# Performance work log

Hardware: AMD Instinct MI355X
Metric: run time of the kernel (lower is better)

## Reference

```python
import jax, jax.numpy as jnp
import numpy as np

VOCAB = 50000
EMBED = 512
COMP = 300
B, L = 2048, 200
CENTER = jnp.array([40.7127, -74.0059], dtype=jnp.float32)


def setup_inputs() -> dict:
    key = jax.random.key(0)
    ks = jax.random.split(key, 8)
    words = jax.random.randint(ks[0], (B, L), 0, VOCAB, dtype=jnp.int64)
    features = jax.random.normal(ks[1], (B, 2), dtype=jnp.float32)
    mask = jnp.ones((B, L), dtype=jnp.float32)
    # nn.Linear(vocab_size, embedding_dim): weight [out, in]
    lim1 = 1.0 / np.sqrt(VOCAB)
    W_hidden = jax.random.uniform(ks[2], (EMBED, VOCAB), jnp.float32, -lim1, lim1)
    b_hidden = jax.random.uniform(ks[3], (EMBED,), jnp.float32, -lim1, lim1)
    lim2 = 1.0 / np.sqrt(EMBED)
    W_pi = jax.random.uniform(ks[4], (COMP, EMBED), jnp.float32, -lim2, lim2)
    b_pi = jax.random.uniform(ks[5], (COMP,), jnp.float32, -lim2, lim2)
    # mu = (rand-0.5)*4 + CENTER ; sigma = rand * log(0.01)
    mu = (jax.random.uniform(ks[6], (COMP, 2), jnp.float32) - 0.5) * 4.0 + CENTER
    sigma = jax.random.uniform(ks[7], (COMP, 2), jnp.float32) * np.log(0.01).astype(np.float32)
    return {"words": words, "features": features, "mask": mask,
            "W_hidden": W_hidden, "b_hidden": b_hidden,
            "W_pi": W_pi, "b_pi": b_pi, "mu": mu, "sigma": sigma}


def reference(words, features, mask, W_hidden, b_hidden, W_pi, b_pi, mu, sigma):
    bsz = words.shape[0]
    # binary bag-of-words one-hot: s[words[i]] = 1 (duplicates collapse to 1)
    q = jnp.zeros((bsz, VOCAB), dtype=W_hidden.dtype)
    q = q.at[jnp.arange(bsz)[:, None], words].set(1.0)
    hidden = jnp.tanh(q @ W_hidden.T + b_hidden)          # [B, E]
    pi = jax.nn.softmax(hidden @ W_pi.T + b_pi, axis=-1).T  # [C, B]
    sigma_out = jnp.exp(sigma)                             # [C, 2]
    return pi, sigma_out, mu
```

## Files before the change

kernel.cpp:

```cpp
#include <hip/hip_runtime.h>
#include <cstdint>
#include <cstddef>

#define VOCAB 50000
#define EMBED 512
#define COMP  300
#define LW    200
#define LPAD  208
#define NCHUNK 8
#define CHUNK_ROWS 50048
#define CHUNK_BYTES ((size_t)CHUNK_ROWS * 64)
#define CPAD  320
#define NPART 80

#define QINVSCALE 28398.0633f
#define QSCALE    3.52136689e-05f

__global__ __launch_bounds__(256) void quant_chunk_kernel(
    const float* __restrict__ in, unsigned char* __restrict__ out)
{
    __shared__ float tile[64 * 68];
    const int cc = blockIdx.x;
    const int wBase = blockIdx.y * 64;
    const int eBase = cc * 64;
    const int t = threadIdx.x;

    {
        const int col4 = t & 15;
        const int w = wBase + col4 * 4;
#pragma unroll
        for (int rr = 0; rr < 4; ++rr) {
            const int el = (t >> 4) + rr * 16;
            float4 v = make_float4(0.f, 0.f, 0.f, 0.f);
            if (w < VOCAB)
                v = *(const float4*)&in[(size_t)(eBase + el) * VOCAB + w];
            const int sw = (col4 * 4 + 8 * ((el >> 4) & 3)) & 63;
            *(float4*)&tile[el * 68 + sw] = v;
        }
    }
    __syncthreads();

    {
        const int wl = t >> 2;
        const int g = t & 3;
        unsigned int pk[4];
#pragma unroll
        for (int q4 = 0; q4 < 4; ++q4) {
            unsigned int p = 0;
#pragma unroll
            for (int k = 0; k < 4; ++k) {
                const int e = g * 16 + q4 * 4 + k;
                const float f = tile[e * 68 + ((wl + 8 * g) & 63)];
                int q = __float2int_rn(f * QINVSCALE) + 128;
                q = q < 0 ? 0 : (q > 255 ? 255 : q);
                p |= (unsigned int)q << (8 * k);
            }
            pk[q4] = p;
        }
        uint4 v = make_uint4(pk[0], pk[1], pk[2], pk[3]);
        *(uint4*)(out + (size_t)cc * CHUNK_BYTES + (size_t)(wBase + wl) * 64 + g * 16) = v;
    }
}

__global__ __launch_bounds__(256) void wpi_tail_kernel(
    const float* __restrict__ W_pi, const float* __restrict__ mu,
    const float* __restrict__ sigma, float* __restrict__ Wtp,
    float* __restrict__ out_tail)
{
    __shared__ float tile[32 * 33];
    const int kBase = blockIdx.x * 32;
    const int cBase = blockIdx.y * 32;
    const int t = threadIdx.x;

    {
        const int cr = t >> 3;
        const int k4 = t & 7;
        float4 v = make_float4(0.f, 0.f, 0.f, 0.f);
        if (cBase + cr < COMP)
            v = *(const float4*)&W_pi[(size_t)(cBase + cr) * EMBED + kBase + k4 * 4];
        tile[cr * 33 + k4 * 4 + 0] = v.x;
        tile[cr * 33 + k4 * 4 + 1] = v.y;
        tile[cr * 33 + k4 * 4 + 2] = v.z;
        tile[cr * 33 + k4 * 4 + 3] = v.w;
    }
    __syncthreads();
    {
        const int kr = t >> 3;
        const int c4 = t & 7;
        float4 v;
        v.x = tile[(c4 * 4 + 0) * 33 + kr];
        v.y = tile[(c4 * 4 + 1) * 33 + kr];
        v.z = tile[(c4 * 4 + 2) * 33 + kr];
        v.w = tile[(c4 * 4 + 3) * 33 + kr];
        *(float4*)&Wtp[(size_t)(kBase + kr) * CPAD + cBase + c4 * 4] = v;
    }
    if (blockIdx.x == 0 && blockIdx.y == 0) {
        for (int tt = t; tt < 2 * COMP; tt += 256) {
            out_tail[tt]            = expf(sigma[tt]);
            out_tail[2 * COMP + tt] = mu[tt];
        }
    }
}

__global__ __launch_bounds__(256) void dedup_kernel(
    const int* __restrict__ words, int* __restrict__ soff)
{
    __shared__ int sw[LW];
    const int i = blockIdx.x;
    const int t = threadIdx.x;
    if (t < LW) sw[t] = words[(size_t)i * LW + t];
    __syncthreads();
    if (t < LPAD) {
        int off = VOCAB * 64;
        if (t < LW) {
            const int w = sw[t];
            int dup = 0;
            for (int j = 0; j < t; ++j) dup |= (sw[j] == w);
            off = (dup ? VOCAB : w) * 64;
        }
        soff[(size_t)i * LPAD + t] = off;
    }
}

__global__ __launch_bounds__(256) void gather_kernel(
    const int* __restrict__ soff, const unsigned char* __restrict__ W8,
    const float* __restrict__ b_hidden, float* __restrict__ h)
{
    __shared__ int sOff[4 * LPAD];
    __shared__ float part[4][256];
    const int b = blockIdx.x;
    const int c = b & 7;
    const int ip = b >> 3;
    const int i0 = ip * 4;
    const int t = threadIdx.x;
    const int w4 = t >> 6, lane = t & 63;

    if (t < LPAD) {
#pragma unroll
        for (int r = 0; r < 4; ++r)
            sOff[r * LPAD + t] = soff[(size_t)(i0 + r) * LPAD + t];
    }
    __syncthreads();

    const unsigned char* base = W8 + (size_t)c * CHUNK_BYTES + (lane & 15) * 4;
    const int j = lane >> 4;
    const int l0 = w4 * 52;
    float ac[4][4];
#pragma unroll
    for (int r = 0; r < 4; ++r)
#pragma unroll
        for (int q = 0; q < 4; ++q) ac[r][q] = 0.f;

#pragma unroll
    for (int s = 0; s < 13; ++s) {
#pragma unroll
        for (int r = 0; r < 4; ++r) {
            const int off = sOff[r * LPAD + l0 + s * 4 + j];
            const unsigned int d = *(const unsigned int*)(base + (unsigned int)off);
            ac[r][0] += (float)(d & 0xffu);
            ac[r][1] += (float)((d >> 8) & 0xffu);
            ac[r][2] += (float)((d >> 16) & 0xffu);
            ac[r][3] += (float)(d >> 24);
        }
    }
#pragma unroll
    for (int r = 0; r < 4; ++r) {
#pragma unroll
        for (int q = 0; q < 4; ++q) {
            ac[r][q] += __shfl_xor(ac[r][q], 16);
            ac[r][q] += __shfl_xor(ac[r][q], 32);
        }
        if (lane < 16)
            *(float4*)&part[r][w4 * 64 + lane * 4] =
                make_float4(ac[r][0], ac[r][1], ac[r][2], ac[r][3]);
    }
    __syncthreads();

    {
        const int r = w4, d = lane;
        const float S = part[r][d] + part[r][64 + d] + part[r][128 + d] + part[r][192 + d];
        const int e = c * 64 + d;
        h[(size_t)(i0 + r) * EMBED + e] = tanhf((S - 26624.0f) * QSCALE + b_hidden[e]);
    }
}

__global__ __launch_bounds__(256) void htrans_kernel(
    const float* __restrict__ h, float* __restrict__ hT, int B)
{
    __shared__ float tile[64 * 65];
    const int i0 = blockIdx.x * 64;
    const int k0 = blockIdx.y * 64;
    const int t = threadIdx.x;
    const int col4 = t & 15;
    const int row = t >> 4;

#pragma unroll
    for (int rr = 0; rr < 4; ++rr) {
        const int r = row + rr * 16;
        const float4 v = *(const float4*)&h[(size_t)(i0 + r) * EMBED + k0 + col4 * 4];
        tile[r * 65 + col4 * 4 + 0] = v.x;
        tile[r * 65 + col4 * 4 + 1] = v.y;
        tile[r * 65 + col4 * 4 + 2] = v.z;
        tile[r * 65 + col4 * 4 + 3] = v.w;
    }
    __syncthreads();
#pragma unroll
    for (int rr = 0; rr < 4; ++rr) {
        const int kr = row + rr * 16;
        float4 v;
        v.x = tile[(col4 * 4 + 0) * 65 + kr];
        v.y = tile[(col4 * 4 + 1) * 65 + kr];
        v.z = tile[(col4 * 4 + 2) * 65 + kr];
        v.w = tile[(col4 * 4 + 3) * 65 + kr];
        *(float4*)&hT[(size_t)(k0 + kr) * B + i0 + col4 * 4] = v;
    }
}

__global__ __launch_bounds__(256) void logits_kernel(
    const float* __restrict__ hT, const float* __restrict__ Wtp,
    const float* __restrict__ b_pi, float* __restrict__ logit,
    float* __restrict__ pm, float* __restrict__ pl, int B)
{
    __shared__ float wt[512 * 16];
    __shared__ float sh[64 * 128];
    const int i0 = blockIdx.x * 128;
    const int cblk = blockIdx.y;
    const int c0base = cblk * 16;
    const int t = threadIdx.x;
    const int wv = __builtin_amdgcn_readfirstlane(t >> 6);
    const int lane = t & 63;

#pragma unroll
    for (int p = 0; p < 8; ++p) {
        const int q = p * 256 + t;
        const int k = q >> 2;
        const int c4 = q & 3;
        *(float4*)&wt[k * 16 + c4 * 4] =
            *(const float4*)&Wtp[(size_t)k * CPAD + c0base + c4 * 4];
    }

    float acc[8] = {0.f, 0.f, 0.f, 0.f, 0.f, 0.f, 0.f, 0.f};

    for (int ks = 0; ks < EMBED; ks += 64) {
        __syncthreads();
#pragma unroll
        for (int p = 0; p < 8; ++p) {
            const int q = p * 256 + t;
            const int k = q >> 5;
            const int f4 = q & 31;
            *(float4*)&sh[k * 128 + f4 * 4] =
                *(const float4*)&hT[(size_t)(ks + k) * B + i0 + f4 * 4];
        }
        __syncthreads();

#pragma unroll 8
        for (int k = 0; k < 64; ++k) {
            const float4 w = *(const float4*)&wt[(ks + k) * 16 + wv * 4];
            const float h0 = sh[k * 128 + lane];
            const float h1 = sh[k * 128 + 64 + lane];
            acc[0] = fmaf(h0, w.x, acc[0]);
            acc[1] = fmaf(h0, w.y, acc[1]);
            acc[2] = fmaf(h0, w.z, acc[2]);
            acc[3] = fmaf(h0, w.w, acc[3]);
            acc[4] = fmaf(h1, w.x, acc[4]);
            acc[5] = fmaf(h1, w.y, acc[5]);
            acc[6] = fmaf(h1, w.z, acc[6]);
            acc[7] = fmaf(h1, w.w, acc[7]);
        }
    }

    float v0[4], v1[4];
    float m0 = -INFINITY, m1 = -INFINITY;
#pragma unroll
    for (int q = 0; q < 4; ++q) {
        const int cc = c0base + wv * 4 + q;
        const float bp = (cc < COMP) ? b_pi[cc] : 0.f;
        v0[q] = acc[q] + bp;
        v1[q] = acc[4 + q] + bp;
        if (cc < COMP) {
            logit[(size_t)cc * B + i0 + lane] = v0[q];
            logit[(size_t)cc * B + i0 + 64 + lane] = v1[q];
            m0 = fmaxf(m0, v0[q]);
            m1 = fmaxf(m1, v1[q]);
        }
    }
    float l0 = 0.f, l1 = 0.f;
#pragma unroll
    for (int q = 0; q < 4; ++q) {
        if (c0base + wv * 4 + q < COMP) {
            l0 += __expf(v0[q] - m0);
            l1 += __expf(v1[q] - m1);
        }
    }
    const int g = cblk * 4 + wv;
    pm[(size_t)g * B + i0 + lane] = m0;
    pl[(size_t)g * B + i0 + lane] = l0;
    pm[(size_t)g * B + i0 + 64 + lane] = m1;
    pl[(size_t)g * B + i0 + 64 + lane] = l1;
}

__global__ __launch_bounds__(64) void softmax_kernel(
    const float* __restrict__ logit, const float* __restrict__ pm,
    const float* __restrict__ pl, float* __restrict__ pi_out, int B)
{
    const int i = blockIdx.x * 64 + threadIdx.x;
    const int part = blockIdx.y;
    float M = -INFINITY;
#pragma unroll 8
    for (int g = 0; g < NPART; ++g) M = fmaxf(M, pm[(size_t)g * B + i]);
    float L = 0.f;
#pragma unroll 8
    for (int g = 0; g < NPART; ++g)
        L += pl[(size_t)g * B + i] * __expf(pm[(size_t)g * B + i] - M);
    const float inv = 1.0f / L;
    const int cEnd = part * 75 + 75;
#pragma unroll 5
    for (int c = part * 75; c < cEnd; ++c) {
        const float x = logit[(size_t)c * B + i];
        pi_out[(size_t)c * B + i] = __expf(x - M) * inv;
    }
}

extern "C" void kernel_launch(void* const* d_in, const int* in_sizes, int n_in,
                              void* d_out, int out_size, void* d_ws, size_t ws_size,
                              hipStream_t stream) {
    const int*   words    = (const int*)d_in[0];
    const float* W_hidden = (const float*)d_in[3];
    const float* b_hidden = (const float*)d_in[4];
    const float* W_pi     = (const float*)d_in[5];
    const float* b_pi     = (const float*)d_in[6];
    const float* mu       = (const float*)d_in[7];
    const float* sigma    = (const float*)d_in[8];
    float* out = (float*)d_out;

    const int B = in_sizes[0] / LW;

    unsigned char* W8   = (unsigned char*)d_ws;
    int*   soff  = (int*)(W8 + NCHUNK * CHUNK_BYTES);
    float* h     = (float*)(soff + (size_t)B * LPAD);
    float* hT    = h  + (size_t)B * EMBED;
    float* Wtp   = hT + (size_t)EMBED * B;
    float* logit = Wtp + (size_t)EMBED * CPAD;
    float* pm    = logit + (size_t)COMP * B;
    float* pl    = pm + (size_t)NPART * B;

    hipLaunchKernelGGL(quant_chunk_kernel, dim3(NCHUNK, CHUNK_ROWS / 64), dim3(256),
                       0, stream, W_hidden, W8);
    hipLaunchKernelGGL(wpi_tail_kernel, dim3(EMBED / 32, CPAD / 32), dim3(256),
                       0, stream, W_pi, mu, sigma, Wtp, out + (size_t)COMP * B);
    hipLaunchKernelGGL(dedup_kernel, dim3(B), dim3(256), 0, stream, words, soff);
    hipLaunchKernelGGL(gather_kernel, dim3((B / 4) * NCHUNK), dim3(256), 0, stream,
                       soff, W8, b_hidden, h);
    hipLaunchKernelGGL(htrans_kernel, dim3(B / 64, EMBED / 64), dim3(256),
                       0, stream, h, hT, B);
    hipLaunchKernelGGL(logits_kernel, dim3(B / 128, 20), dim3(256), 0, stream,
                       hT, Wtp, b_pi, logit, pm, pl, B);
    hipLaunchKernelGGL(softmax_kernel, dim3(B / 64, 4), dim3(64), 0, stream,
                       logit, pm, pl, out, B);
}
```

Measured before the change: 254.7 us.

## Fuse W_pi and h transposes into logits kernel, drop two transpose launches

Removes the separate W_pi transpose and h transpose kernels. The logits kernel now reads W_pi and h in their native row-major layouts and transposes them while staging into shared memory, using an XOR swizzle on the h tile to limit bank conflicts. The sigma/mu tail output moves into the dedup kernel. This saves two kernel launches and the extra global round trips through hT and Wtp. In exchange, the shared-memory stores become scalar and strided, and W_pi is reloaded from global memory by every block.

```diff
diff --git a/kernel.cpp b/kernel.cpp
--- a/kernel.cpp
+++ b/kernel.cpp
@@ -10,7 +10,6 @@
 #define NCHUNK 8
 #define CHUNK_ROWS 50048
 #define CHUNK_BYTES ((size_t)CHUNK_ROWS * 64)
-#define CPAD  320
 #define NPART 80
 
 #define QINVSCALE 28398.0633f
@@ -62,48 +61,10 @@
     }
 }
 
-__global__ __launch_bounds__(256) void wpi_tail_kernel(
-    const float* __restrict__ W_pi, const float* __restrict__ mu,
-    const float* __restrict__ sigma, float* __restrict__ Wtp,
+__global__ __launch_bounds__(256) void dedup_kernel(
+    const int* __restrict__ words, int* __restrict__ soff,
+    const float* __restrict__ mu, const float* __restrict__ sigma,
     float* __restrict__ out_tail)
-{
-    __shared__ float tile[32 * 33];
-    const int kBase = blockIdx.x * 32;
-    const int cBase = blockIdx.y * 32;
-    const int t = threadIdx.x;
-
-    {
-        const int cr = t >> 3;
-        const int k4 = t & 7;
-        float4 v = make_float4(0.f, 0.f, 0.f, 0.f);
-        if (cBase + cr < COMP)
-            v = *(const float4*)&W_pi[(size_t)(cBase + cr) * EMBED + kBase + k4 * 4];
-        tile[cr * 33 + k4 * 4 + 0] = v.x;
-        tile[cr * 33 + k4 * 4 + 1] = v.y;
-        tile[cr * 33 + k4 * 4 + 2] = v.z;
-        tile[cr * 33 + k4 * 4 + 3] = v.w;
-    }
-    __syncthreads();
-    {
-        const int kr = t >> 3;
-        const int c4 = t & 7;
-        float4 v;
-        v.x = tile[(c4 * 4 + 0) * 33 + kr];
-        v.y = tile[(c4 * 4 + 1) * 33 + kr];
-        v.z = tile[(c4 * 4 + 2) * 33 + kr];
-        v.w = tile[(c4 * 4 + 3) * 33 + kr];
-        *(float4*)&Wtp[(size_t)(kBase + kr) * CPAD + cBase + c4 * 4] = v;
-    }
-    if (blockIdx.x == 0 && blockIdx.y == 0) {
-        for (int tt = t; tt < 2 * COMP; tt += 256) {
-            out_tail[tt]            = expf(sigma[tt]);
-            out_tail[2 * COMP + tt] = mu[tt];
-        }
-    }
-}
-
-__global__ __launch_bounds__(256) void dedup_kernel(
-    const int* __restrict__ words, int* __restrict__ soff)
 {
     __shared__ int sw[LW];
     const int i = blockIdx.x;
@@ -120,6 +81,12 @@
         }
         soff[(size_t)i * LPAD + t] = off;
     }
+    if (i == 0) {
+        for (int tt = t; tt < 2 * COMP; tt += 256) {
+            out_tail[tt]            = expf(sigma[tt]);
+            out_tail[2 * COMP + tt] = mu[tt];
+        }
+    }
 }
 
 __global__ __launch_bounds__(256) void gather_kernel(
@@ -184,40 +151,8 @@
     }
 }
 
-__global__ __launch_bounds__(256) void htrans_kernel(
-    const float* __restrict__ h, float* __restrict__ hT, int B)
-{
-    __shared__ float tile[64 * 65];
-    const int i0 = blockIdx.x * 64;
-    const int k0 = blockIdx.y * 64;
-    const int t = threadIdx.x;
-    const int col4 = t & 15;
-    const int row = t >> 4;
-
-#pragma unroll
-    for (int rr = 0; rr < 4; ++rr) {
-        const int r = row + rr * 16;
-        const float4 v = *(const float4*)&h[(size_t)(i0 + r) * EMBED + k0 + col4 * 4];
-        tile[r * 65 + col4 * 4 + 0] = v.x;
-        tile[r * 65 + col4 * 4 + 1] = v.y;
-        tile[r * 65 + col4 * 4 + 2] = v.z;
-        tile[r * 65 + col4 * 4 + 3] = v.w;
-    }
-    __syncthreads();
-#pragma unroll
-    for (int rr = 0; rr < 4; ++rr) {
-        const int kr = row + rr * 16;
-        float4 v;
-        v.x = tile[(col4 * 4 + 0) * 65 + kr];
-        v.y = tile[(col4 * 4 + 1) * 65 + kr];
-        v.z = tile[(col4 * 4 + 2) * 65 + kr];
-        v.w = tile[(col4 * 4 + 3) * 65 + kr];
-        *(float4*)&hT[(size_t)(k0 + kr) * B + i0 + col4 * 4] = v;
-    }
-}
-
 __global__ __launch_bounds__(256) void logits_kernel(
-    const float* __restrict__ hT, const float* __restrict__ Wtp,
+    const float* __restrict__ h, const float* __restrict__ W_pi,
     const float* __restrict__ b_pi, float* __restrict__ logit,
     float* __restrict__ pm, float* __restrict__ pl, int B)
 {
@@ -233,10 +168,16 @@
 #pragma unroll
     for (int p = 0; p < 8; ++p) {
         const int q = p * 256 + t;
-        const int k = q >> 2;
-        const int c4 = q & 3;
-        *(float4*)&wt[k * 16 + c4 * 4] =
-            *(const float4*)&Wtp[(size_t)k * CPAD + c0base + c4 * 4];
+        const int cl = q & 15;
+        const int k4 = q >> 4;
+        const int c = c0base + cl;
+        float4 v = make_float4(0.f, 0.f, 0.f, 0.f);
+        if (c < COMP)
+            v = *(const float4*)&W_pi[(size_t)c * EMBED + k4 * 4];
+        wt[(k4 * 4 + 0) * 16 + cl] = v.x;
+        wt[(k4 * 4 + 1) * 16 + cl] = v.y;
+        wt[(k4 * 4 + 2) * 16 + cl] = v.z;
+        wt[(k4 * 4 + 3) * 16 + cl] = v.w;
     }
 
     float acc[8] = {0.f, 0.f, 0.f, 0.f, 0.f, 0.f, 0.f, 0.f};
@@ -246,18 +187,24 @@
 #pragma unroll
         for (int p = 0; p < 8; ++p) {
             const int q = p * 256 + t;
-            const int k = q >> 5;
-            const int f4 = q & 31;
-            *(float4*)&sh[k * 128 + f4 * 4] =
-                *(const float4*)&hT[(size_t)(ks + k) * B + i0 + f4 * 4];
+            const int row = q >> 4;
+            const int k4 = q & 15;
+            const float4 v =
+                *(const float4*)&h[(size_t)(i0 + row) * EMBED + ks + k4 * 4];
+            const int swz = row ^ ((k4 & 7) << 2);
+            sh[(k4 * 4 + 0) * 128 + swz] = v.x;
+            sh[(k4 * 4 + 1) * 128 + swz] = v.y;
+            sh[(k4 * 4 + 2) * 128 + swz] = v.z;
+            sh[(k4 * 4 + 3) * 128 + swz] = v.w;
         }
         __syncthreads();
 
 #pragma unroll 8
         for (int k = 0; k < 64; ++k) {
             const float4 w = *(const float4*)&wt[(ks + k) * 16 + wv * 4];
-            const float h0 = sh[k * 128 + lane];
-            const float h1 = sh[k * 128 + 64 + lane];
+            const int col = lane ^ (((k >> 2) & 7) << 2);
+            const float h0 = sh[k * 128 + col];
+            const float h1 = sh[k * 128 + 64 + col];
             acc[0] = fmaf(h0, w.x, acc[0]);
             acc[1] = fmaf(h0, w.y, acc[1]);
             acc[2] = fmaf(h0, w.z, acc[2]);
@@ -338,23 +285,18 @@
     unsigned char* W8   = (unsigned char*)d_ws;
     int*   soff  = (int*)(W8 + NCHUNK * CHUNK_BYTES);
     float* h     = (float*)(soff + (size_t)B * LPAD);
-    float* hT    = h  + (size_t)B * EMBED;
-    float* Wtp   = hT + (size_t)EMBED * B;
-    float* logit = Wtp + (size_t)EMBED * CPAD;
+    float* logit = h + (size_t)B * EMBED;
     float* pm    = logit + (size_t)COMP * B;
     float* pl    = pm + (size_t)NPART * B;
 
     hipLaunchKernelGGL(quant_chunk_kernel, dim3(NCHUNK, CHUNK_ROWS / 64), dim3(256),
                        0, stream, W_hidden, W8);
-    hipLaunchKernelGGL(wpi_tail_kernel, dim3(EMBED / 32, CPAD / 32), dim3(256),
-                       0, stream, W_pi, mu, sigma, Wtp, out + (size_t)COMP * B);
-    hipLaunchKernelGGL(dedup_kernel, dim3(B), dim3(256), 0, stream, words, soff);
+    hipLaunchKernelGGL(dedup_kernel, dim3(B), dim3(256), 0, stream,
+                       words, soff, mu, sigma, out + (size_t)COMP * B);
     hipLaunchKernelGGL(gather_kernel, dim3((B / 4) * NCHUNK), dim3(256), 0, stream,
                        soff, W8, b_hidden, h);
-    hipLaunchKernelGGL(htrans_kernel, dim3(B / 64, EMBED / 64), dim3(256),
-                       0, stream, h, hT, B);
     hipLaunchKernelGGL(logits_kernel, dim3(B / 128, 20), dim3(256), 0, stream,
-                       hT, Wtp, b_pi, logit, pm, pl, B);
+                       h, W_pi, b_pi, logit, pm, pl, B);
     hipLaunchKernelGGL(softmax_kernel, dim3(B / 64, 4), dim3(64), 0, stream,
                        logit, pm, pl, out, B);
 }
```

Result: no change. 250.4 us (-1.7%).
